# Kernel optimization log

Hardware: AMD Instinct MI355X
Metric: run time of the kernel (lower is better)

Reference implementation:

```python
import math
import jax, jax.numpy as jnp
import numpy as np

B, L, DM, D, C = 8, 2048, 512, 512, 2
K_TOP = int(math.floor(C * math.log(L)))  # floor(c * log L) = 15


def setup_inputs() -> dict:
    key = jax.random.key(0)
    ks = jax.random.split(key, 9)
    s = 0.02
    return {
        "Q": jax.random.normal(ks[0], (B, L, DM), jnp.float32),
        "K": jax.random.normal(ks[1], (B, L, DM), jnp.float32),
        "V": jax.random.normal(ks[2], (B, L, DM), jnp.float32),
        "WQ_w": jax.random.normal(ks[3], (DM, D), jnp.float32) * s,
        "WQ_b": jnp.zeros((D,), jnp.float32),
        "WK_w": jax.random.normal(ks[4], (DM, D), jnp.float32) * s,
        "WK_b": jnp.zeros((D,), jnp.float32),
        "WV_w": jax.random.normal(ks[5], (DM, D), jnp.float32) * s,
        "WV_b": jnp.zeros((D,), jnp.float32),
    }


def reference(Q, K, V, WQ_w, WQ_b, WK_w, WK_b, WV_w, WV_b):
    Bn, Ln, _ = Q.shape
    # K/V truncated (zero-padded if shorter) to length L; here S == L.
    Kc = K[:, :Ln, :]
    Vc = V[:, :Ln, :]
    # Dense projections
    q = Q @ WQ_w + WQ_b    # [B, L, d]
    k = Kc @ WK_w + WK_b   # [B, L, d]
    v = Vc @ WV_w + WV_b   # [B, L, d]
    # FFT-based autocorrelation along the time axis
    Qf = jnp.fft.rfft(q, axis=1)
    Kf = jnp.fft.rfft(k, axis=1)
    Rxx = jnp.fft.irfft(Qf * jnp.conjugate(Kf), n=Ln, axis=1)  # [B, L, d]
    # Top-k lag selection per (batch, channel)
    Rl = jnp.moveaxis(Rxx, 1, -1)                # [B, d, L]
    Wk, Ik = jax.lax.top_k(Rl, K_TOP)            # [B, d, k]
    Wk = jax.nn.softmax(Wk, axis=-1)
    # Weighted aggregation of time-rolled values: roll(v, -i)[t] = v[(t+i) % L]
    vl = jnp.moveaxis(v, 1, -1)                  # [B, d, L]
    t = jnp.arange(Ln)
    idx = (t[None, None, None, :] + Ik[..., None]) % Ln   # [B, d, k, L]
    rolled = jnp.take_along_axis(vl[:, :, None, :], idx, axis=-1)  # [B, d, k, L]
    A = jnp.einsum('bdk,bdkl->bld', Wk, rolled)  # [B, L, d]
    return A
```

## Files before the change

### kernel.cpp

```cpp
#include <hip/hip_runtime.h>
#include <hip/hip_bf16.h>
#include <math.h>

#define Bz 8
#define Lz 2048
#define Dz 512
#define KTOP 15

typedef __attribute__((ext_vector_type(8))) unsigned short ushort8x;
typedef __attribute__((ext_vector_type(8))) _Float16 half8x;
typedef __attribute__((ext_vector_type(4))) float floatx4;
typedef __attribute__((ext_vector_type(16))) float float16x;

__global__ __launch_bounds__(256) void wtrans3(
    const float* __restrict__ w0, const float* __restrict__ w1,
    const float* __restrict__ w2, _Float16* __restrict__ t0,
    _Float16* __restrict__ t1, _Float16* __restrict__ t2) {
  const float* w = blockIdx.z == 0 ? w0 : (blockIdx.z == 1 ? w1 : w2);
  _Float16* t = blockIdx.z == 0 ? t0 : (blockIdx.z == 1 ? t1 : t2);
  __shared__ float tile[32][33];
  const int n0 = blockIdx.x * 32, k0 = blockIdx.y * 32;
  const int tx = threadIdx.x, ty = threadIdx.y;
  #pragma unroll
  for (int i = 0; i < 4; ++i)
    tile[ty + 8 * i][tx] = w[(size_t)(k0 + ty + 8 * i) * Dz + n0 + tx];
  __syncthreads();
  #pragma unroll
  for (int i = 0; i < 4; ++i)
    t[(size_t)(n0 + ty + 8 * i) * Dz + k0 + tx] = (_Float16)tile[tx][ty + 8 * i];
}

#define ALDA 40
__global__ __launch_bounds__(256) void gemm3(
    const float* __restrict__ A0, const float* __restrict__ A1,
    const float* __restrict__ A2, const _Float16* __restrict__ B0,
    const _Float16* __restrict__ B1, const _Float16* __restrict__ B2,
    const float* __restrict__ c0, const float* __restrict__ c1,
    const float* __restrict__ c2, _Float16* __restrict__ o0,
    _Float16* __restrict__ o1, _Float16* __restrict__ o2) {
  const int K = Dz;
  const int z = blockIdx.z;
  const float* A = z == 0 ? A0 : (z == 1 ? A1 : A2);
  const _Float16* Bt = z == 0 ? B0 : (z == 1 ? B1 : B2);
  const float* bias = z == 0 ? c0 : (z == 1 ? c1 : c2);
  _Float16* oT = z == 0 ? o0 : (z == 1 ? o1 : o2);

  __shared__ __attribute__((aligned(16))) _Float16 smem[18432];
  _Float16* Asb = smem;
  _Float16* Bsb = smem + 10240;
  const int tid = threadIdx.x;
  const int m0 = blockIdx.y * 128;
  const int n0 = blockIdx.x * 128;
  const int lane = tid & 63;
  const int wv = tid >> 6;
  const int wr = wv & 1, wc = wv >> 1;
  const int ln = lane & 15;
  const int quad = lane >> 4;

  floatx4 acc[4][4];
  #pragma unroll
  for (int i = 0; i < 4; ++i)
    #pragma unroll
    for (int j = 0; j < 4; ++j) acc[i][j] = (floatx4){0.f, 0.f, 0.f, 0.f};

  float4 ra4[4];

  #pragma unroll
  for (int j = 0; j < 4; ++j) {
    const int slot = tid + 256 * j;
    const int r = slot >> 3, c4 = slot & 7;
    ra4[j] = *(const float4*)&A[(size_t)(m0 + r) * K + 4 * c4];
  }
  #pragma unroll
  for (int jj = 0; jj < 2; ++jj) {
    const int s = tid + 256 * jj;
    const int row = s >> 2;
    const int qs = (s & 3) ^ (row & 3);
    const unsigned short* src =
        (const unsigned short*)Bt + (size_t)(n0 + row) * K + 8 * qs;
    __builtin_amdgcn_global_load_lds(
        (const __attribute__((address_space(1))) unsigned int*)src,
        (__attribute__((address_space(3))) unsigned int*)&Bsb[(jj * 256 + wv * 64) * 8],
        16, 0, 0);
  }
  #pragma unroll
  for (int j = 0; j < 4; ++j) {
    const int slot = tid + 256 * j;
    const int r = slot >> 3, c4 = slot & 7;
    union { _Float16 h[4]; unsigned long long u; } p;
    p.h[0] = (_Float16)ra4[j].x;
    p.h[1] = (_Float16)ra4[j].y;
    p.h[2] = (_Float16)ra4[j].z;
    p.h[3] = (_Float16)ra4[j].w;
    *(unsigned long long*)&Asb[r * ALDA + 4 * c4] = p.u;
  }
  __syncthreads();

  const int NKT = K / 32;
  for (int kt = 0; kt < NKT; ++kt) {
    const int cur = kt & 1;
    const int nxt = cur ^ 1;
    if (kt + 1 < NKT) {
      const int kof = (kt + 1) * 32;
      #pragma unroll
      for (int j = 0; j < 4; ++j) {
        const int slot = tid + 256 * j;
        const int r = slot >> 3, c4 = slot & 7;
        ra4[j] = *(const float4*)&A[(size_t)(m0 + r) * K + kof + 4 * c4];
      }
      #pragma unroll
      for (int jj = 0; jj < 2; ++jj) {
        const int s = tid + 256 * jj;
        const int row = s >> 2;
        const int qs = (s & 3) ^ (row & 3);
        const unsigned short* src =
            (const unsigned short*)Bt + (size_t)(n0 + row) * K + kof + 8 * qs;
        __builtin_amdgcn_global_load_lds(
            (const __attribute__((address_space(1))) unsigned int*)src,
            (__attribute__((address_space(3))) unsigned int*)
                &Bsb[nxt * 4096 + (jj * 256 + wv * 64) * 8],
            16, 0, 0);
      }
    }
    const _Float16* As = Asb + cur * 5120;
    const _Float16* Bs = Bsb + cur * 4096;
    half8x af[4], bf[4];
    #pragma unroll
    for (int i = 0; i < 4; ++i)
      af[i] = *(const half8x*)&As[(wr * 64 + 16 * i + ln) * ALDA + 8 * quad];
    #pragma unroll
    for (int j = 0; j < 4; ++j) {
      const int row = wc * 64 + 16 * j + ln;
      bf[j] = *(const half8x*)&Bs[row * 32 + 8 * (quad ^ (ln & 3))];
    }
    #pragma unroll
    for (int i = 0; i < 4; ++i)
      #pragma unroll
      for (int j = 0; j < 4; ++j)
        acc[i][j] = __builtin_amdgcn_mfma_f32_16x16x32_f16(af[i], bf[j], acc[i][j], 0, 0, 0);
    if (kt + 1 < NKT) {
      _Float16* Asw = Asb + nxt * 5120;
      #pragma unroll
      for (int j = 0; j < 4; ++j) {
        const int slot = tid + 256 * j;
        const int r = slot >> 3, c4 = slot & 7;
        union { _Float16 h[4]; unsigned long long u; } p;
        p.h[0] = (_Float16)ra4[j].x;
        p.h[1] = (_Float16)ra4[j].y;
        p.h[2] = (_Float16)ra4[j].z;
        p.h[3] = (_Float16)ra4[j].w;
        *(unsigned long long*)&Asw[r * ALDA + 4 * c4] = p.u;
      }
      __syncthreads();
    }
  }

  const int bb = m0 >> 11;
  const int l0 = m0 & 2047;
  #pragma unroll
  for (int j = 0; j < 4; ++j) {
    const int d = n0 + wc * 64 + 16 * j + ln;
    const float bv = bias[d];
    _Float16* op = oT + (size_t)(bb * Dz + d) * Lz + l0 + wr * 64 + 4 * quad;
    #pragma unroll
    for (int i = 0; i < 4; ++i) {
      union { _Float16 h[4]; unsigned long long u; } p;
      #pragma unroll
      for (int r = 0; r < 4; ++r) p.h[r] = (_Float16)(acc[i][j][r] + bv);
      *(unsigned long long*)(op + 16 * i) = p.u;
    }
  }
}

#define QXS 2072

__device__ __forceinline__ int swz128(int byte) {
  return byte ^ (((byte >> 7) & 7) << 4);
}

__global__ __launch_bounds__(256) void corr_mfma_topk(
    const _Float16* __restrict__ qT, const _Float16* __restrict__ kT,
    float* __restrict__ Wk, int* __restrict__ Ik) {
  __shared__ __attribute__((aligned(16))) unsigned short qx[8 * QXS];
  __shared__ __attribute__((aligned(16))) unsigned short ke[Lz];
  __shared__ float cv[64];
  __shared__ int ci[64];

  const int tid = threadIdx.x;
  const size_t chan = (size_t)blockIdx.x * Lz;
  const unsigned short* qg = (const unsigned short*)(qT + chan);
  const unsigned short* kg = (const unsigned short*)(kT + chan);

  {
    ushort8x v = *(const ushort8x*)(kg + 8 * tid);
    *(ushort8x*)((char*)ke + swz128(16 * tid)) = v;
  }
  for (int c = tid; c < QXS / 8; c += 256) {
    union { unsigned int d[8]; ushort8x v[2]; } b;
    b.v[0] = *(const ushort8x*)(qg + ((8 * c) & (Lz - 1)));
    b.v[1] = *(const ushort8x*)(qg + ((8 * c + 8) & (Lz - 1)));
    #pragma unroll
    for (int s = 0; s < 8; ++s) {
      union { unsigned int d[4]; ushort8x v; } w;
      if (s & 1) {
        #pragma unroll
        for (int t = 0; t < 4; ++t)
          w.d[t] = __builtin_amdgcn_alignbit(b.d[(s >> 1) + t + 1],
                                             b.d[(s >> 1) + t], 16);
      } else {
        #pragma unroll
        for (int t = 0; t < 4; ++t) w.d[t] = b.d[(s >> 1) + t];
      }
      *(ushort8x*)&qx[s * QXS + 8 * c] = w.v;
    }
  }
  __syncthreads();

  const int lane = tid & 63;
  const int wv = tid >> 6;
  const int jb = lane & 31;
  const int hi = lane >> 5;
  const char* aptr = (const char*)qx + (jb & 7) * (2 * QXS) + 16 * (jb >> 3) + 16 * hi;
  const int bb2 = ((8 * hi - 32 * jb) & (Lz - 1)) * 2;

  float16x acc0 = {0.f, 0.f, 0.f, 0.f, 0.f, 0.f, 0.f, 0.f,
                   0.f, 0.f, 0.f, 0.f, 0.f, 0.f, 0.f, 0.f};
  float16x acc1 = acc0;

  const int t0base = wv << 9;
  #pragma unroll 4
  for (int it = 0; it < 32; ++it) {
    const int t2 = 2 * (t0base + 16 * it);
    half8x a = *(const half8x*)(aptr + t2);
    const int y0 = (bb2 + t2) & (2 * Lz - 1);
    const int y1 = (y0 + 2048) & (2 * Lz - 1);
    half8x b0 = *(const half8x*)((const char*)ke + swz128(y0));
    half8x b1 = *(const half8x*)((const char*)ke + swz128(y1));
    acc0 = __builtin_amdgcn_mfma_f32_32x32x16_f16(a, b0, acc0, 0, 0, 0);
    acc1 = __builtin_amdgcn_mfma_f32_32x32x16_f16(a, b1, acc1, 0, 0, 0);
  }

  __syncthreads();
  float* red = (float*)qx;
  {
    const int rbase = wv * 8192;
    #pragma unroll
    for (int g = 0; g < 4; ++g) {
      const int tau0 = 8 * g + 4 * hi + 32 * jb;
      float4 p0, p1;
      p0.x = acc0[4 * g + 0]; p0.y = acc0[4 * g + 1];
      p0.z = acc0[4 * g + 2]; p0.w = acc0[4 * g + 3];
      p1.x = acc1[4 * g + 0]; p1.y = acc1[4 * g + 1];
      p1.z = acc1[4 * g + 2]; p1.w = acc1[4 * g + 3];
      *(float4*)((char*)red + swz128(rbase + 4 * tau0)) = p0;
      *(float4*)((char*)red + swz128(rbase + 4 * (tau0 + 1024))) = p1;
    }
  }
  __syncthreads();

  float vals[8] = {0.f, 0.f, 0.f, 0.f, 0.f, 0.f, 0.f, 0.f};
  {
    const char* rb = (const char*)red;
    #pragma unroll
    for (int w = 0; w < 4; ++w) {
      float4 a0 = *(const float4*)(rb + swz128(w * 8192 + 32 * tid));
      float4 a1 = *(const float4*)(rb + swz128(w * 8192 + 32 * tid + 16));
      vals[0] += a0.x; vals[1] += a0.y; vals[2] += a0.z; vals[3] += a0.w;
      vals[4] += a1.x; vals[5] += a1.y; vals[6] += a1.z; vals[7] += a1.w;
    }
  }

  unsigned key[8];
  #pragma unroll
  for (int j = 0; j < 8; ++j) {
    const unsigned u = __float_as_uint(vals[j]);
    key[j] = u ^ (unsigned)(((int)u >> 31) | 0x80000000);
  }
  unsigned p = 0;
  for (int b = 31; b >= 0; --b) {
    const unsigned c = p | (1u << b);
    int cnt = 0;
    #pragma unroll
    for (int j = 0; j < 8; ++j)
      cnt += __popcll(__ballot(key[j] >= c));
    if (cnt >= KTOP) p = c;
  }
  const unsigned long long ltm = (1ull << lane) - 1ull;
  int base = 0;
  #pragma unroll
  for (int j = 0; j < 8; ++j) {
    const bool g = key[j] > p;
    const unsigned long long m = __ballot(g);
    const int pos = base + __popcll(m & ltm);
    if (g) { cv[wv * KTOP + pos] = vals[j]; ci[wv * KTOP + pos] = 8 * tid + j; }
    base += __popcll(m);
  }
  #pragma unroll
  for (int j = 0; j < 8; ++j) {
    const bool e = (key[j] == p);
    const unsigned long long m = __ballot(e);
    const int pos = base + __popcll(m & ltm);
    if (e && pos < KTOP) { cv[wv * KTOP + pos] = vals[j]; ci[wv * KTOP + pos] = 8 * tid + j; }
    base += __popcll(m);
  }
  __syncthreads();

  if (wv == 0) {
    const bool act = lane < 4 * KTOP;
    const float v = act ? cv[lane] : 0.f;
    const int ti = act ? ci[lane] : 0;
    unsigned k2 = 0;
    if (act) {
      const unsigned u = __float_as_uint(v);
      k2 = u ^ (unsigned)(((int)u >> 31) | 0x80000000);
    }
    unsigned pp = 0;
    for (int b = 31; b >= 0; --b) {
      const unsigned c = pp | (1u << b);
      if (__popcll(__ballot(k2 >= c)) >= KTOP) pp = c;
    }
    const unsigned long long mg = __ballot(k2 > pp);
    const int tot = __popcll(mg);
    bool sel = (k2 > pp);
    int pos = __popcll(mg & ltm);
    const unsigned long long me = __ballot(k2 == pp);
    const int pose = tot + __popcll(me & ltm);
    if (k2 == pp && pose < KTOP) { sel = true; pos = pose; }
    if (sel) { cv[pos] = v; ci[pos] = ti; }
    const float sv = (lane < KTOP) ? cv[lane] : -3.0e38f;
    const int si = (lane < KTOP) ? ci[lane] : 0;
    float gm = sv;
    #pragma unroll
    for (int off = 1; off < 64; off <<= 1)
      gm = fmaxf(gm, __shfl_xor(gm, off, 64));
    float e = (lane < KTOP) ? expf(sv - gm) : 0.f;
    float es = e;
    #pragma unroll
    for (int off = 1; off < 64; off <<= 1) es += __shfl_xor(es, off, 64);
    if (lane < KTOP) {
      const size_t ob = (size_t)blockIdx.x * KTOP;
      Wk[ob + lane] = e / es;
      Ik[ob + lane] = si;
    }
  }
}

#define GSWZ(b) ((b) ^ ((((b) >> 12) & 7) << 4))

__global__ __launch_bounds__(256) void gather_fused(
    const _Float16* __restrict__ vT, const float* __restrict__ Wk,
    const int* __restrict__ Ik, float* __restrict__ out) {
  __shared__ __attribute__((aligned(16))) _Float16 ls[8 * Lz];
  __shared__ float os[256 * 9];
  const int tid = threadIdx.x;
  const int d0 = blockIdx.x * 8;
  const int b = blockIdx.y;
  float* ob = out + (size_t)b * Lz * Dz;

  const char* lsb = (const char*)ls;
  #pragma unroll
  for (int it = 0; it < 8; ++it) {
    const int slot = tid + 256 * it;
    const int dl2 = slot >> 8, c = slot & 255;
    ushort8x v = *(const ushort8x*)((const unsigned short*)vT +
                                    ((size_t)(b * Dz + d0 + dl2) * Lz) + 8 * c);
    *(ushort8x*)((char*)ls + GSWZ(16 * slot)) = v;
  }

  const int dl = tid & 7;
  const int lg = tid >> 3;
  const size_t wb = ((size_t)b * Dz + d0 + dl) * KTOP;
  float wreg[KTOP];
  int ireg[KTOP];
  #pragma unroll
  for (int k = 0; k < KTOP; ++k) {
    wreg[k] = Wk[wb + k];
    ireg[k] = Ik[wb + k];
  }
  __syncthreads();

  const int rowb = dl * 4096;
  for (int lt = 0; lt < 8; ++lt) {
    const int lbase = lt * 256 + lg * 8;
    float acc[8] = {0.f, 0.f, 0.f, 0.f, 0.f, 0.f, 0.f, 0.f};
    for (int k = 0; k < KTOP; ++k) {
      const float w = wreg[k];
      const int p = (lbase + ireg[k]) & (Lz - 1);
      const int b0 = p >> 3;
      const int b1 = (b0 + 1) & 255;
      union { ushort8x v; unsigned d[4]; } A0, A1;
      A0.v = *(const ushort8x*)(lsb + GSWZ(rowb + 16 * b0));
      A1.v = *(const ushort8x*)(lsb + GSWZ(rowb + 16 * b1));
      const int h = p & 7;
      unsigned e0, e1, e2, e3, e4, e5;
      if (h & 4) { e0 = A0.d[2]; e1 = A0.d[3]; e2 = A1.d[0]; e3 = A1.d[1]; e4 = A1.d[2]; e5 = A1.d[3]; }
      else       { e0 = A0.d[0]; e1 = A0.d[1]; e2 = A0.d[2]; e3 = A0.d[3]; e4 = A1.d[0]; e5 = A1.d[1]; }
      unsigned f0, f1, f2, f3, f4;
      if (h & 2) { f0 = e1; f1 = e2; f2 = e3; f3 = e4; f4 = e5; }
      else       { f0 = e0; f1 = e1; f2 = e2; f3 = e3; f4 = e4; }
      const int sh = (h & 1) << 4;
      unsigned o0 = __builtin_amdgcn_alignbit(f1, f0, sh);
      unsigned o1 = __builtin_amdgcn_alignbit(f2, f1, sh);
      unsigned o2 = __builtin_amdgcn_alignbit(f3, f2, sh);
      unsigned o3 = __builtin_amdgcn_alignbit(f4, f3, sh);
      union { unsigned u; _Float16 hh[2]; } c0, c1, c2, c3;
      c0.u = o0; c1.u = o1; c2.u = o2; c3.u = o3;
      acc[0] += w * (float)c0.hh[0]; acc[1] += w * (float)c0.hh[1];
      acc[2] += w * (float)c1.hh[0]; acc[3] += w * (float)c1.hh[1];
      acc[4] += w * (float)c2.hh[0]; acc[5] += w * (float)c2.hh[1];
      acc[6] += w * (float)c3.hh[0]; acc[7] += w * (float)c3.hh[1];
    }
    __syncthreads();
    #pragma unroll
    for (int j = 0; j < 8; ++j) os[(lg * 8 + j) * 9 + dl] = acc[j];
    __syncthreads();
    #pragma unroll
    for (int c2 = 0; c2 < 2; ++c2) {
      const int sl = tid + 256 * c2;
      const int l = sl >> 1, c = sl & 1;
      float4 o;
      o.x = os[l * 9 + 4 * c + 0];
      o.y = os[l * 9 + 4 * c + 1];
      o.z = os[l * 9 + 4 * c + 2];
      o.w = os[l * 9 + 4 * c + 3];
      *(float4*)&ob[(size_t)(lt * 256 + l) * Dz + d0 + 4 * c] = o;
    }
  }
}

extern "C" void kernel_launch(void* const* d_in, const int* in_sizes, int n_in,
                              void* d_out, int out_size, void* d_ws, size_t ws_size,
                              hipStream_t stream) {
  const float* Q = (const float*)d_in[0];
  const float* K = (const float*)d_in[1];
  const float* V = (const float*)d_in[2];
  const float* WQw = (const float*)d_in[3];
  const float* WQb = (const float*)d_in[4];
  const float* WKw = (const float*)d_in[5];
  const float* WKb = (const float*)d_in[6];
  const float* WVw = (const float*)d_in[7];
  const float* WVb = (const float*)d_in[8];
  float* out = (float*)d_out;

  const size_t CH = (size_t)Bz * Dz;
  const size_t NEL = (size_t)Bz * Lz * Dz;

  char* ws = (char*)d_ws;
  _Float16* qT = (_Float16*)ws;
  _Float16* kT = qT + NEL;
  _Float16* vT = kT + NEL;
  _Float16* WQt = vT + NEL;
  _Float16* WKt = WQt + (size_t)Dz * Dz;
  _Float16* WVt = WKt + (size_t)Dz * Dz;
  float* Wk = (float*)(WVt + (size_t)Dz * Dz);
  int* Ik = (int*)(Wk + CH * KTOP);

  dim3 tr_block(32, 8);

  wtrans3<<<dim3(16, 16, 3), tr_block, 0, stream>>>(WQw, WKw, WVw, WQt, WKt, WVt);

  gemm3<<<dim3(Dz / 128, (Bz * Lz) / 128, 3), dim3(256), 0, stream>>>(
      Q, K, V, WQt, WKt, WVt, WQb, WKb, WVb, qT, kT, vT);

  corr_mfma_topk<<<dim3((unsigned)CH), dim3(256), 0, stream>>>(qT, kT, Wk, Ik);

  gather_fused<<<dim3(Dz / 8, Bz), dim3(256), 0, stream>>>(vT, Wk, Ik, out);
}
```

Measured before the change: 272.1 us.

## Retile projection GEMM to 64x512 tiles with LDS-staged coalesced output

The projection GEMM now uses 64-row by full-512-column tiles instead of 128x128 tiles. Each block reads its fp32 A rows once rather than four times across N-tiles, which cuts global traffic on the large activation inputs. The epilogue stages the transposed fp16 outputs through LDS so that stores to the [B,D,L] layout are 16-byte coalesced. In exchange, LDS use grows to about 74KB per block, each wave holds a larger accumulator array, and the B tiles are streamed through LDS by every block.

```diff
diff --git a/kernel.cpp b/kernel.cpp
--- a/kernel.cpp
+++ b/kernel.cpp
@@ -31,7 +31,7 @@
 }
 
 #define ALDA 40
-__global__ __launch_bounds__(256) void gemm3(
+__global__ __launch_bounds__(256, 2) void gemm3(
     const float* __restrict__ A0, const float* __restrict__ A1,
     const float* __restrict__ A2, const _Float16* __restrict__ B0,
     const _Float16* __restrict__ B1, const _Float16* __restrict__ B2,
@@ -39,52 +39,51 @@
     const float* __restrict__ c2, _Float16* __restrict__ o0,
     _Float16* __restrict__ o1, _Float16* __restrict__ o2) {
   const int K = Dz;
-  const int z = blockIdx.z;
+  const int z = blockIdx.y;
   const float* A = z == 0 ? A0 : (z == 1 ? A1 : A2);
   const _Float16* Bt = z == 0 ? B0 : (z == 1 ? B1 : B2);
   const float* bias = z == 0 ? c0 : (z == 1 ? c1 : c2);
   _Float16* oT = z == 0 ? o0 : (z == 1 ? o1 : o2);
 
-  __shared__ __attribute__((aligned(16))) _Float16 smem[18432];
+  __shared__ __attribute__((aligned(16))) _Float16 smem[37888];
   _Float16* Asb = smem;
-  _Float16* Bsb = smem + 10240;
+  _Float16* Bsb = smem + 5120;
   const int tid = threadIdx.x;
-  const int m0 = blockIdx.y * 128;
-  const int n0 = blockIdx.x * 128;
+  const int m0 = blockIdx.x * 64;
   const int lane = tid & 63;
   const int wv = tid >> 6;
-  const int wr = wv & 1, wc = wv >> 1;
   const int ln = lane & 15;
   const int quad = lane >> 4;
 
-  floatx4 acc[4][4];
+  floatx4 acc[4][8];
   #pragma unroll
   for (int i = 0; i < 4; ++i)
     #pragma unroll
-    for (int j = 0; j < 4; ++j) acc[i][j] = (floatx4){0.f, 0.f, 0.f, 0.f};
-
-  float4 ra4[4];
-
-  #pragma unroll
-  for (int j = 0; j < 4; ++j) {
+    for (int j = 0; j < 8; ++j) acc[i][j] = (floatx4){0.f, 0.f, 0.f, 0.f};
+
+  float4 ra4[2];
+
+  #pragma unroll
+  for (int j = 0; j < 2; ++j) {
     const int slot = tid + 256 * j;
     const int r = slot >> 3, c4 = slot & 7;
     ra4[j] = *(const float4*)&A[(size_t)(m0 + r) * K + 4 * c4];
   }
   #pragma unroll
-  for (int jj = 0; jj < 2; ++jj) {
-    const int s = tid + 256 * jj;
-    const int row = s >> 2;
-    const int qs = (s & 3) ^ (row & 3);
+  for (int jj = 0; jj < 8; ++jj) {
+    const int g = jj * 256 + tid;
+    const int row = g >> 2;
+    const int qs = (g & 3) ^ (row & 3);
     const unsigned short* src =
-        (const unsigned short*)Bt + (size_t)(n0 + row) * K + 8 * qs;
+        (const unsigned short*)Bt + (size_t)row * K + 8 * qs;
     __builtin_amdgcn_global_load_lds(
         (const __attribute__((address_space(1))) unsigned int*)src,
-        (__attribute__((address_space(3))) unsigned int*)&Bsb[(jj * 256 + wv * 64) * 8],
+        (__attribute__((address_space(3))) unsigned int*)
+            &Bsb[(jj * 256 + wv * 64) * 8],
         16, 0, 0);
   }
   #pragma unroll
-  for (int j = 0; j < 4; ++j) {
+  for (int j = 0; j < 2; ++j) {
     const int slot = tid + 256 * j;
     const int r = slot >> 3, c4 = slot & 7;
     union { _Float16 h[4]; unsigned long long u; } p;
@@ -103,45 +102,43 @@
     if (kt + 1 < NKT) {
       const int kof = (kt + 1) * 32;
       #pragma unroll
-      for (int j = 0; j < 4; ++j) {
+      for (int j = 0; j < 2; ++j) {
         const int slot = tid + 256 * j;
         const int r = slot >> 3, c4 = slot & 7;
         ra4[j] = *(const float4*)&A[(size_t)(m0 + r) * K + kof + 4 * c4];
       }
       #pragma unroll
-      for (int jj = 0; jj < 2; ++jj) {
-        const int s = tid + 256 * jj;
-        const int row = s >> 2;
-        const int qs = (s & 3) ^ (row & 3);
+      for (int jj = 0; jj < 8; ++jj) {
+        const int g = jj * 256 + tid;
+        const int row = g >> 2;
+        const int qs = (g & 3) ^ (row & 3);
         const unsigned short* src =
-            (const unsigned short*)Bt + (size_t)(n0 + row) * K + kof + 8 * qs;
+            (const unsigned short*)Bt + (size_t)row * K + kof + 8 * qs;
         __builtin_amdgcn_global_load_lds(
             (const __attribute__((address_space(1))) unsigned int*)src,
             (__attribute__((address_space(3))) unsigned int*)
-                &Bsb[nxt * 4096 + (jj * 256 + wv * 64) * 8],
+                &Bsb[nxt * 16384 + (jj * 256 + wv * 64) * 8],
             16, 0, 0);
       }
     }
-    const _Float16* As = Asb + cur * 5120;
-    const _Float16* Bs = Bsb + cur * 4096;
-    half8x af[4], bf[4];
+    const _Float16* As = Asb + cur * 2560;
+    const _Float16* Bs = Bsb + cur * 16384;
+    half8x af[4];
     #pragma unroll
     for (int i = 0; i < 4; ++i)
-      af[i] = *(const half8x*)&As[(wr * 64 + 16 * i + ln) * ALDA + 8 * quad];
-    #pragma unroll
-    for (int j = 0; j < 4; ++j) {
-      const int row = wc * 64 + 16 * j + ln;
-      bf[j] = *(const half8x*)&Bs[row * 32 + 8 * (quad ^ (ln & 3))];
-    }
-    #pragma unroll
-    for (int i = 0; i < 4; ++i)
+      af[i] = *(const half8x*)&As[(16 * i + ln) * ALDA + 8 * quad];
+    #pragma unroll
+    for (int j = 0; j < 8; ++j) {
+      const int row = wv * 128 + 16 * j + ln;
+      half8x bf = *(const half8x*)&Bs[row * 32 + 8 * (quad ^ (ln & 3))];
       #pragma unroll
-      for (int j = 0; j < 4; ++j)
-        acc[i][j] = __builtin_amdgcn_mfma_f32_16x16x32_f16(af[i], bf[j], acc[i][j], 0, 0, 0);
+      for (int i = 0; i < 4; ++i)
+        acc[i][j] = __builtin_amdgcn_mfma_f32_16x16x32_f16(af[i], bf, acc[i][j], 0, 0, 0);
+    }
     if (kt + 1 < NKT) {
-      _Float16* Asw = Asb + nxt * 5120;
+      _Float16* Asw = Asb + nxt * 2560;
       #pragma unroll
-      for (int j = 0; j < 4; ++j) {
+      for (int j = 0; j < 2; ++j) {
         const int slot = tid + 256 * j;
         const int r = slot >> 3, c4 = slot & 7;
         union { _Float16 h[4]; unsigned long long u; } p;
@@ -155,20 +152,29 @@
     }
   }
 
-  const int bb = m0 >> 11;
-  const int l0 = m0 & 2047;
-  #pragma unroll
-  for (int j = 0; j < 4; ++j) {
-    const int d = n0 + wc * 64 + 16 * j + ln;
-    const float bv = bias[d];
-    _Float16* op = oT + (size_t)(bb * Dz + d) * Lz + l0 + wr * 64 + 4 * quad;
+  __syncthreads();
+  _Float16* TB = smem;
+  #pragma unroll
+  for (int j = 0; j < 8; ++j) {
+    const int n_l = wv * 128 + 16 * j + ln;
+    const float bv = bias[n_l];
     #pragma unroll
     for (int i = 0; i < 4; ++i) {
       union { _Float16 h[4]; unsigned long long u; } p;
       #pragma unroll
       for (int r = 0; r < 4; ++r) p.h[r] = (_Float16)(acc[i][j][r] + bv);
-      *(unsigned long long*)(op + 16 * i) = p.u;
-    }
+      *(unsigned long long*)&TB[n_l * 72 + 16 * i + 4 * quad] = p.u;
+    }
+  }
+  __syncthreads();
+  const int bb = m0 >> 11;
+  const int l0 = m0 & 2047;
+  #pragma unroll
+  for (int it = 0; it < 16; ++it) {
+    const int slot = tid + 256 * it;
+    const int d = slot >> 3, c = slot & 7;
+    *(ushort8x*)(oT + ((size_t)(bb * Dz + d)) * Lz + l0 + 8 * c) =
+        *(const ushort8x*)&TB[d * 72 + 8 * c];
   }
 }
 
@@ -459,7 +465,7 @@
 
   wtrans3<<<dim3(16, 16, 3), tr_block, 0, stream>>>(WQw, WKw, WVw, WQt, WKt, WVt);
 
-  gemm3<<<dim3(Dz / 128, (Bz * Lz) / 128, 3), dim3(256), 0, stream>>>(
+  gemm3<<<dim3((Bz * Lz) / 64, 3), dim3(256), 0, stream>>>(
       Q, K, V, WQt, WKt, WVt, WQb, WKb, WVb, qT, kT, vT);
 
   corr_mfma_topk<<<dim3((unsigned)CH), dim3(256), 0, stream>>>(qT, kT, Wk, Ik);
```

New measurement: 268.2 us. No clear change (-1.4%).
